# Kernel optimization log

Measured on AMD Instinct MI355X. Metric: run time of the kernel, lower is better.

Reference implementation:

```python
import jax, jax.numpy as jnp
import numpy as np

WINDOW_SIZE = 11
SIGMA = 1.5
C1 = 0.01 ** 2
C2 = 0.03 ** 2


def _gaussian_window(channel, dtype):
    # 1D gaussian, normalized, then outer product -> 2D window [ws, ws]
    center = WINDOW_SIZE // 2
    x = jnp.arange(WINDOW_SIZE, dtype=jnp.float32) - center
    g = jnp.exp(-(x ** 2) / (2.0 * SIGMA ** 2))
    g = g / g.sum()
    w2d = jnp.outer(g, g)  # [ws, ws]
    # depthwise kernel: [C_out=channel, C_in/groups=1, ws, ws]
    return jnp.broadcast_to(w2d, (channel, 1, WINDOW_SIZE, WINDOW_SIZE)).astype(dtype)


def _depthwise_blur(x, window):
    pad = WINDOW_SIZE // 2
    return jax.lax.conv_general_dilated(
        x, window,
        window_strides=(1, 1),
        padding=[(pad, pad), (pad, pad)],
        feature_group_count=x.shape[1],
        dimension_numbers=('NCHW', 'OIHW', 'NCHW'))


def setup_inputs() -> dict:
    key = jax.random.key(0)
    k1, k2 = jax.random.split(key)
    img1 = jax.random.uniform(k1, (16, 3, 512, 512), dtype=jnp.float32)
    img2 = jax.random.uniform(k2, (16, 3, 512, 512), dtype=jnp.float32)
    return {"img1": img1, "img2": img2}


def reference(img1, img2):
    channel = img1.shape[1]
    window = _gaussian_window(channel, img1.dtype)

    mu1 = _depthwise_blur(img1, window)
    mu2 = _depthwise_blur(img2, window)
    mu1_sq = mu1 * mu1
    mu2_sq = mu2 * mu2
    mu1_mu2 = mu1 * mu2

    sigma1_sq = _depthwise_blur(img1 * img1, window) - mu1_sq
    sigma2_sq = _depthwise_blur(img2 * img2, window) - mu2_sq
    sigma12 = _depthwise_blur(img1 * img2, window) - mu1_mu2

    ssim_map = ((2.0 * mu1_mu2 + C1) * (2.0 * sigma12 + C2)) / (
        (mu1_sq + mu2_sq + C1) * (sigma1_sq + sigma2_sq + C2))
    return ssim_map.mean()  # size_average=True
```

## Files before the change

### kernel.cpp

```cpp
#include <hip/hip_runtime.h>


typedef _Float16 f16;
typedef __attribute__((ext_vector_type(4))) _Float16 f16x4;
typedef __attribute__((ext_vector_type(8))) _Float16 f16x8;
typedef __attribute__((ext_vector_type(4))) float f32x4;

#define IMGW 512
#define IMGH 512
#define NPL 48
#define NBLOCKS (NPL * 8 * 8)
#define NPIX 12582912.0
#define REDT 1024

#define SRW 84
#define PROWS 80
#define IMGOFFD (PROWS * SRW)

#define INV_T 0.99967202f

__device__ const float G_dev[11] = {0.00102838f, 0.00759876f, 0.03600077f,
                                    0.10936069f, 0.21300554f, 0.26601172f,
                                    0.21300554f, 0.10936069f, 0.03600077f,
                                    0.00759876f, 0.00102838f};

__global__ __launch_bounds__(256, 3) void ssim_main(const float* __restrict__ img1,
                                                    const float* __restrict__ img2,
                                                    float* __restrict__ partial) {
    __shared__ __align__(16) float sP[2 * IMGOFFD];
    __shared__ float wsum[4];

    const int tid  = threadIdx.x;
    const int lane = tid & 63;
    const int wv   = tid >> 6;
    const int l15  = lane & 15;
    const int lg   = lane >> 4;

    const int bid   = blockIdx.x;
    const int plane = bid >> 6;
    const int rem   = bid & 63;
    const int by    = rem >> 3;
    const int bx    = rem & 7;
    const int R0    = by * 64 - 5;
    const int AC0   = bx * 64 - 8;

    const float* __restrict__ p1 = img1 + (size_t)plane * (IMGH * IMGW);
    const float* __restrict__ p2 = img2 + (size_t)plane * (IMGH * IMGW);

    const int rlo = (R0 < 0) ? -R0 : 0;
    const int rhi = (R0 + 74 > IMGH) ? (IMGH - R0) : 74;
    const int llo = (AC0 < 0) ? ((-AC0 + 3) >> 2) : 0;
    const int lhic = (IMGW - AC0) >> 2;
    const int lhi = (lhic < 20) ? lhic : 20;
    const bool edge = (rlo != 0) | (rhi != 74) | (llo != 0) | (lhi != 20);

    if (edge) {
        for (int it = 0; it < 27; ++it) {
            const int i = tid + it * 256;
            if (i < 6720) *(float2*)&sP[2 * i] = make_float2(0.0f, 0.0f);
        }
        __syncthreads();
    } else {
        #pragma unroll
        for (int it = 0; it < 2; ++it) {
            const int i = tid + it * 256;
            if (i < 504) {
                const int im = (i >= 252) ? 1 : 0;
                const int k  = i - im * 252;
                *(float2*)&sP[im * IMGOFFD + 74 * SRW + 2 * k] = make_float2(0.0f, 0.0f);
            }
        }
    }

    {
        const int nr = rhi - rlo;
        for (int L = wv; L < 2 * nr; L += 4) {
            const int im  = (L >= nr) ? 1 : 0;
            const int row = rlo + (L - im * nr);
            const float* __restrict__ bp = im ? p2 : p1;
            float* lp = &sP[im * IMGOFFD + row * SRW];
            if (lane >= llo && lane < lhi) {
                const float* gp = bp + (size_t)(R0 + row) * IMGW + (AC0 + 4 * lane);
                __builtin_amdgcn_global_load_lds(gp, lp, 16, 0, 0);
            }
        }
    }
    __syncthreads();

    f16x8 bband;
    #pragma unroll
    for (int j = 0; j < 8; ++j) {
        const int kj = (j < 4) ? (4 * lg + j) : (16 + 4 * lg + (j - 4));
        const int t  = kj - l15;
        const float w = (t >= 0 && t < 11) ? G_dev[t] : 0.0f;
        bband[j] = (f16)w;
    }

    const f32x4 zero4 = {0.0f, 0.0f, 0.0f, 0.0f};

    f16x4 hv[5][5];
    #pragma unroll
    for (int t = 0; t < 5; ++t) {
        int p = 3 + 16 * t + l15;
        if (t == 4) p = (p > PROWS - 1) ? PROWS - 1 : p;
        const int ro = 16 * wv + 4 * lg;
        const float* __restrict__ b1 = &sP[ro * SRW + p];
        const float* __restrict__ b2 = &sP[IMGOFFD + ro * SRW + p];
        f16x8 fx, fy;
        #pragma unroll
        for (int e = 0; e < 4; ++e) {
            fx[e]     = (f16)b1[e * SRW];
            fx[e + 4] = (f16)b1[(16 + e) * SRW];
            fy[e]     = (f16)b2[e * SRW];
            fy[e + 4] = (f16)b2[(16 + e) * SRW];
        }
        const f16x8 fxx = fx * fx;
        const f16x8 fyy = fy * fy;
        const f16x8 fxy = fx * fy;

        const f32x4 dx  = __builtin_amdgcn_mfma_f32_16x16x32_f16(fx,  bband, zero4, 0, 0, 0);
        const f32x4 dy  = __builtin_amdgcn_mfma_f32_16x16x32_f16(fy,  bband, zero4, 0, 0, 0);
        const f32x4 dxx = __builtin_amdgcn_mfma_f32_16x16x32_f16(fxx, bband, zero4, 0, 0, 0);
        const f32x4 dyy = __builtin_amdgcn_mfma_f32_16x16x32_f16(fyy, bband, zero4, 0, 0, 0);
        const f32x4 dxy = __builtin_amdgcn_mfma_f32_16x16x32_f16(fxy, bband, zero4, 0, 0, 0);

        hv[t][0] = (f16x4){(f16)dx[0],  (f16)dx[1],  (f16)dx[2],  (f16)dx[3]};
        hv[t][1] = (f16x4){(f16)dy[0],  (f16)dy[1],  (f16)dy[2],  (f16)dy[3]};
        hv[t][2] = (f16x4){(f16)dxx[0], (f16)dxx[1], (f16)dxx[2], (f16)dxx[3]};
        hv[t][3] = (f16x4){(f16)dyy[0], (f16)dyy[1], (f16)dyy[2], (f16)dyy[3]};
        hv[t][4] = (f16x4){(f16)dxy[0], (f16)dxy[1], (f16)dxy[2], (f16)dxy[3]};
    }

    float acc = 0.0f;
    const float C1 = 1.0e-4f;
    const float C2 = 9.0e-4f;
    #pragma unroll
    for (int m = 0; m < 4; ++m) {
        f32x4 h[5];
        #pragma unroll
        for (int q = 0; q < 5; ++q) {
            const f16x8 a = __builtin_shufflevector(hv[m][q], hv[m + 1][q],
                                                    0, 1, 2, 3, 4, 5, 6, 7);
            h[q] = __builtin_amdgcn_mfma_f32_16x16x32_f16(a, bband, zero4, 0, 0, 0);
            h[q] *= INV_T;
        }
        #pragma unroll
        for (int r = 0; r < 4; ++r) {
            const float mu1 = h[0][r], mu2 = h[1][r];
            const float exx = h[2][r], eyy = h[3][r], exy = h[4][r];
            const float mu1s = mu1 * mu1;
            const float mu2s = mu2 * mu2;
            const float mu12 = mu1 * mu2;
            const float s1  = exx - mu1s;
            const float s2  = eyy - mu2s;
            const float s12 = exy - mu12;
            const float num = fmaf(2.0f, mu12, C1) * fmaf(2.0f, s12, C2);
            const float den = (mu1s + mu2s + C1) * (s1 + s2 + C2);
            float rd = __builtin_amdgcn_rcpf(den);
            rd = rd * fmaf(-den, rd, 2.0f);
            acc = fmaf(num, rd, acc);
        }
    }

    #pragma unroll
    for (int off = 32; off > 0; off >>= 1)
        acc += __shfl_down(acc, off, 64);
    if (lane == 0) wsum[wv] = acc;
    __syncthreads();
    if (tid == 0)
        partial[bid] = (wsum[0] + wsum[1]) + (wsum[2] + wsum[3]);
}

__global__ __launch_bounds__(REDT) void ssim_reduce(const float* __restrict__ partial,
                                                    float* __restrict__ out) {
    const int tid = threadIdx.x;
    double s = 0.0;
    for (int i = tid; i < NBLOCKS; i += REDT)
        s += (double)partial[i];
    #pragma unroll
    for (int off = 32; off > 0; off >>= 1)
        s += __shfl_down(s, off, 64);
    __shared__ double wsd[REDT / 64];
    if ((tid & 63) == 0) wsd[tid >> 6] = s;
    __syncthreads();
    if (tid == 0) {
        double t = 0.0;
        #pragma unroll
        for (int i = 0; i < REDT / 64; ++i) t += wsd[i];
        out[0] = (float)(t / NPIX);
    }
}

extern "C" void kernel_launch(void* const* d_in, const int* in_sizes, int n_in,
                              void* d_out, int out_size, void* d_ws, size_t ws_size,
                              hipStream_t stream) {
    const float* img1 = (const float*)d_in[0];
    const float* img2 = (const float*)d_in[1];
    float* partial = (float*)d_ws;
    float* out = (float*)d_out;
    ssim_main<<<NBLOCKS, 256, 0, stream>>>(img1, img2, partial);
    ssim_reduce<<<1, REDT, 0, stream>>>(partial, out);
}
```

Before: 57.01 us.

## Swap blur pass order to use vectorized row reads from LDS

Reorders the separable blur so the first MFMA pass filters horizontally along rows, using a shifted band matrix, and the second filters vertically. The LDS reads become 16-byte vector loads along rows instead of strided scalar column reads. The shared tile shrinks to the 74 rows actually needed and interior blocks skip zero-fill and bounds logic. The price is recomputing horizontal passes per m-iteration, with two row groups per output group, which adds MFMA work.

Result: faster. 52.16 us (-8.5%).

```diff
diff --git a/kernel.cpp b/kernel.cpp
--- a/kernel.cpp
+++ b/kernel.cpp
@@ -2,7 +2,6 @@
 
 
 typedef _Float16 f16;
-typedef __attribute__((ext_vector_type(4))) _Float16 f16x4;
 typedef __attribute__((ext_vector_type(8))) _Float16 f16x8;
 typedef __attribute__((ext_vector_type(4))) float f32x4;
 
@@ -14,8 +13,8 @@
 #define REDT 1024
 
 #define SRW 84
-#define PROWS 80
-#define IMGOFFD (PROWS * SRW)
+#define PR 74
+#define IMGOFFD (PR * SRW)
 
 #define INV_T 0.99967202f
 
@@ -47,101 +46,108 @@
     const float* __restrict__ p1 = img1 + (size_t)plane * (IMGH * IMGW);
     const float* __restrict__ p2 = img2 + (size_t)plane * (IMGH * IMGW);
 
-    const int rlo = (R0 < 0) ? -R0 : 0;
-    const int rhi = (R0 + 74 > IMGH) ? (IMGH - R0) : 74;
-    const int llo = (AC0 < 0) ? ((-AC0 + 3) >> 2) : 0;
-    const int lhic = (IMGW - AC0) >> 2;
-    const int lhi = (lhic < 20) ? lhic : 20;
-    const bool edge = (rlo != 0) | (rhi != 74) | (llo != 0) | (lhi != 20);
-
-    if (edge) {
-        for (int it = 0; it < 27; ++it) {
+    const bool interior = (by >= 1) & (by <= 6) & (bx >= 1) & (bx <= 6);
+
+    if (interior) {
+        for (int r = wv; r < PR; r += 4) {
+            if (lane < 21) {
+                const float* gp = p1 + (size_t)(R0 + r) * IMGW + (AC0 + 4 * lane);
+                __builtin_amdgcn_global_load_lds(gp, &sP[r * SRW], 16, 0, 0);
+            }
+        }
+        for (int r = wv; r < PR; r += 4) {
+            if (lane < 21) {
+                const float* gp = p2 + (size_t)(R0 + r) * IMGW + (AC0 + 4 * lane);
+                __builtin_amdgcn_global_load_lds(gp, &sP[IMGOFFD + r * SRW], 16, 0, 0);
+            }
+        }
+    } else {
+        for (int it = 0; it < 25; ++it) {
             const int i = tid + it * 256;
-            if (i < 6720) *(float2*)&sP[2 * i] = make_float2(0.0f, 0.0f);
+            if (i < IMGOFFD) ((float2*)sP)[i] = make_float2(0.0f, 0.0f);
         }
         __syncthreads();
-    } else {
-        #pragma unroll
-        for (int it = 0; it < 2; ++it) {
-            const int i = tid + it * 256;
-            if (i < 504) {
-                const int im = (i >= 252) ? 1 : 0;
-                const int k  = i - im * 252;
-                *(float2*)&sP[im * IMGOFFD + 74 * SRW + 2 * k] = make_float2(0.0f, 0.0f);
-            }
-        }
-    }
-
-    {
-        const int nr = rhi - rlo;
-        for (int L = wv; L < 2 * nr; L += 4) {
-            const int im  = (L >= nr) ? 1 : 0;
-            const int row = rlo + (L - im * nr);
-            const float* __restrict__ bp = im ? p2 : p1;
-            float* lp = &sP[im * IMGOFFD + row * SRW];
+        const int rlo = (R0 < 0) ? -R0 : 0;
+        const int rhi = (R0 + PR > IMGH) ? (IMGH - R0) : PR;
+        const int llo = (AC0 < 0) ? ((-AC0) >> 2) : 0;
+        const int lhiT = (IMGW - AC0) >> 2;
+        const int lhi = (lhiT < 21) ? lhiT : 21;
+        for (int r = rlo + wv; r < rhi; r += 4) {
             if (lane >= llo && lane < lhi) {
-                const float* gp = bp + (size_t)(R0 + row) * IMGW + (AC0 + 4 * lane);
-                __builtin_amdgcn_global_load_lds(gp, lp, 16, 0, 0);
+                const float* gp = p1 + (size_t)(R0 + r) * IMGW + (AC0 + 4 * lane);
+                __builtin_amdgcn_global_load_lds(gp, &sP[r * SRW], 16, 0, 0);
+            }
+        }
+        for (int r = rlo + wv; r < rhi; r += 4) {
+            if (lane >= llo && lane < lhi) {
+                const float* gp = p2 + (size_t)(R0 + r) * IMGW + (AC0 + 4 * lane);
+                __builtin_amdgcn_global_load_lds(gp, &sP[IMGOFFD + r * SRW], 16, 0, 0);
             }
         }
     }
     __syncthreads();
 
-    f16x8 bband;
+    f16x8 bbH, bbV;
     #pragma unroll
     for (int j = 0; j < 8; ++j) {
         const int kj = (j < 4) ? (4 * lg + j) : (16 + 4 * lg + (j - 4));
-        const int t  = kj - l15;
-        const float w = (t >= 0 && t < 11) ? G_dev[t] : 0.0f;
-        bband[j] = (f16)w;
+        const int tH = kj - l15 - 3;
+        const int tV = kj - l15;
+        bbH[j] = (f16)((tH >= 0 && tH < 11) ? G_dev[tH] : 0.0f);
+        bbV[j] = (f16)((tV >= 0 && tV < 11) ? G_dev[tV] : 0.0f);
     }
 
     const f32x4 zero4 = {0.0f, 0.0f, 0.0f, 0.0f};
 
-    f16x4 hv[5][5];
-    #pragma unroll
-    for (int t = 0; t < 5; ++t) {
-        int p = 3 + 16 * t + l15;
-        if (t == 4) p = (p > PROWS - 1) ? PROWS - 1 : p;
-        const int ro = 16 * wv + 4 * lg;
-        const float* __restrict__ b1 = &sP[ro * SRW + p];
-        const float* __restrict__ b2 = &sP[IMGOFFD + ro * SRW + p];
-        f16x8 fx, fy;
-        #pragma unroll
-        for (int e = 0; e < 4; ++e) {
-            fx[e]     = (f16)b1[e * SRW];
-            fx[e + 4] = (f16)b1[(16 + e) * SRW];
-            fy[e]     = (f16)b2[e * SRW];
-            fy[e + 4] = (f16)b2[(16 + e) * SRW];
-        }
-        const f16x8 fxx = fx * fx;
-        const f16x8 fyy = fy * fy;
-        const f16x8 fxy = fx * fy;
-
-        const f32x4 dx  = __builtin_amdgcn_mfma_f32_16x16x32_f16(fx,  bband, zero4, 0, 0, 0);
-        const f32x4 dy  = __builtin_amdgcn_mfma_f32_16x16x32_f16(fy,  bband, zero4, 0, 0, 0);
-        const f32x4 dxx = __builtin_amdgcn_mfma_f32_16x16x32_f16(fxx, bband, zero4, 0, 0, 0);
-        const f32x4 dyy = __builtin_amdgcn_mfma_f32_16x16x32_f16(fyy, bband, zero4, 0, 0, 0);
-        const f32x4 dxy = __builtin_amdgcn_mfma_f32_16x16x32_f16(fxy, bband, zero4, 0, 0, 0);
-
-        hv[t][0] = (f16x4){(f16)dx[0],  (f16)dx[1],  (f16)dx[2],  (f16)dx[3]};
-        hv[t][1] = (f16x4){(f16)dy[0],  (f16)dy[1],  (f16)dy[2],  (f16)dy[3]};
-        hv[t][2] = (f16x4){(f16)dxx[0], (f16)dxx[1], (f16)dxx[2], (f16)dxx[3]};
-        hv[t][3] = (f16x4){(f16)dyy[0], (f16)dyy[1], (f16)dyy[2], (f16)dyy[3]};
-        hv[t][4] = (f16x4){(f16)dxy[0], (f16)dxy[1], (f16)dxy[2], (f16)dxy[3]};
-    }
+    const int rowA = 16 * wv + l15;
+    int rowB = 16 * wv + 16 + l15;
+    if (rowB > PR - 1) rowB = PR - 1;
 
     float acc = 0.0f;
     const float C1 = 1.0e-4f;
     const float C2 = 9.0e-4f;
+
     #pragma unroll
     for (int m = 0; m < 4; ++m) {
+        const int cg = 16 * m + 4 * lg;
+        f32x4 D0[5], D1[5];
+        #pragma unroll
+        for (int s = 0; s < 2; ++s) {
+            const int row = s ? rowB : rowA;
+            const float* __restrict__ r1 = &sP[row * SRW];
+            const float* __restrict__ r2 = &sP[IMGOFFD + row * SRW];
+            const f32x4 xa = *(const f32x4*)&r1[cg];
+            const f32x4 xb = *(const f32x4*)&r1[cg + 16];
+            const f32x4 ya = *(const f32x4*)&r2[cg];
+            const f32x4 yb = *(const f32x4*)&r2[cg + 16];
+            f16x8 fx, fy;
+            #pragma unroll
+            for (int e = 0; e < 4; ++e) {
+                fx[e]     = (f16)xa[e];
+                fx[e + 4] = (f16)xb[e];
+                fy[e]     = (f16)ya[e];
+                fy[e + 4] = (f16)yb[e];
+            }
+            const f16x8 fxx = fx * fx;
+            const f16x8 fyy = fy * fy;
+            const f16x8 fxy = fx * fy;
+            f32x4* D = s ? D1 : D0;
+            D[0] = __builtin_amdgcn_mfma_f32_16x16x32_f16(fx,  bbH, zero4, 0, 0, 0);
+            D[1] = __builtin_amdgcn_mfma_f32_16x16x32_f16(fy,  bbH, zero4, 0, 0, 0);
+            D[2] = __builtin_amdgcn_mfma_f32_16x16x32_f16(fxx, bbH, zero4, 0, 0, 0);
+            D[3] = __builtin_amdgcn_mfma_f32_16x16x32_f16(fyy, bbH, zero4, 0, 0, 0);
+            D[4] = __builtin_amdgcn_mfma_f32_16x16x32_f16(fxy, bbH, zero4, 0, 0, 0);
+        }
         f32x4 h[5];
         #pragma unroll
         for (int q = 0; q < 5; ++q) {
-            const f16x8 a = __builtin_shufflevector(hv[m][q], hv[m + 1][q],
-                                                    0, 1, 2, 3, 4, 5, 6, 7);
-            h[q] = __builtin_amdgcn_mfma_f32_16x16x32_f16(a, bband, zero4, 0, 0, 0);
+            f16x8 av;
+            #pragma unroll
+            for (int j = 0; j < 4; ++j) {
+                av[j]     = (f16)D0[q][j];
+                av[j + 4] = (f16)D1[q][j];
+            }
+            h[q] = __builtin_amdgcn_mfma_f32_16x16x32_f16(av, bbV, zero4, 0, 0, 0);
             h[q] *= INV_T;
         }
         #pragma unroll
```
